# Kernel tuning notes

Hardware: AMD Instinct MI355X
Metric: run time of the kernel (lower is better)

## Reference

```python
import jax, jax.numpy as jnp
import numpy as np

EPS = 1e-5

def _conv1x1(x, w, b):
    # x: (B,C,H,W), w: (O,C), b: (O,)
    return jnp.einsum('bchw,oc->bohw', x, w) + b[None, :, None, None]

def _maxpool2(x):
    B, C, H, W = x.shape
    return x.reshape(B, C, H // 2, 2, W // 2, 2).max(axis=(3, 5))

def setup_inputs() -> dict:
    key = jax.random.key(0)
    ks = jax.random.split(key, 12)
    B, C, Ci, H, W = 8, 256, 128, 64, 64
    s = lambda k, shape, scale: jax.random.normal(k, shape, jnp.float32) * scale
    return {
        'x': s(ks[0], (B, C, H, W), 1.0),
        'neighborFeat': s(ks[1], (B, C, H, W), 1.0),
        'g_w': s(ks[2], (Ci, C), 0.05), 'g_b': jnp.zeros((Ci,), jnp.float32),
        'theta_w': s(ks[3], (Ci, C), 0.05), 'theta_b': jnp.zeros((Ci,), jnp.float32),
        'phi_w': s(ks[4], (Ci, C), 0.05), 'phi_b': jnp.zeros((Ci,), jnp.float32),
        'w_w': s(ks[5], (C, Ci), 0.05), 'w_b': jnp.zeros((C,), jnp.float32),
        'bn_gamma': s(ks[6], (C,), 0.1) + 1.0,
        'bn_beta': s(ks[7], (C,), 0.1),
        'bn_mean': s(ks[8], (C,), 0.1),
        'bn_var': jax.random.uniform(ks[9], (C,), jnp.float32, 0.5, 1.5),
    }

def reference(x, neighborFeat, g_w, g_b, theta_w, theta_b, phi_w, phi_b,
              w_w, w_b, bn_gamma, bn_beta, bn_mean, bn_var):
    B, C, H, W = x.shape
    Ci = g_w.shape[0]
    # g: conv1x1 on x then maxpool2 -> (B, Nkv, Ci)
    g_x = _maxpool2(_conv1x1(x, g_w, g_b)).reshape(B, Ci, -1).transpose(0, 2, 1)
    # theta: conv1x1 on neighborFeat, full res -> (B, Nq, Ci)
    theta_x = _conv1x1(neighborFeat, theta_w, theta_b).reshape(B, Ci, -1).transpose(0, 2, 1)
    # phi: conv1x1 on neighborFeat then maxpool2 -> (B, Ci, Nkv)
    phi_x = _maxpool2(_conv1x1(neighborFeat, phi_w, phi_b)).reshape(B, Ci, -1)
    f = jnp.einsum('bqc,bck->bqk', theta_x, phi_x)       # (B, Nq, Nkv)
    f_div_C = jax.nn.softmax(f, axis=-1)
    y = jnp.einsum('bqk,bkc->bqc', f_div_C, g_x)          # (B, Nq, Ci)
    y = y.transpose(0, 2, 1).reshape(B, Ci, H, W)
    # W: conv1x1 + BatchNorm (eval mode with running stats)
    wy = _conv1x1(y, w_w, w_b)
    wy = (wy - bn_mean[None, :, None, None]) * (bn_gamma[None, :, None, None]
          * jax.lax.rsqrt(bn_var + EPS)[None, :, None, None]) + bn_beta[None, :, None, None]
    return wy + x
```

## Files before the change

kernel.cpp:

```cpp
#include <hip/hip_runtime.h>

typedef __attribute__((ext_vector_type(8))) short short8;
typedef __attribute__((ext_vector_type(4))) short short4v;
typedef __attribute__((ext_vector_type(4))) float f32x4;

__device__ __forceinline__ float bf2f(short s) {
  union { unsigned u; float f; } cv;
  cv.u = ((unsigned)(unsigned short)s) << 16;
  return cv.f;
}
__device__ __forceinline__ short f2bf(float f) {
  union { float f; unsigned u; } cv;
  cv.f = f;
  unsigned r = (cv.u + 0x7fffu + ((cv.u >> 16) & 1u)) >> 16;
  return (short)(unsigned short)r;
}

#define MFMA16(a, b, c) __builtin_amdgcn_mfma_f32_16x16x32_bf16((a), (b), (c), 0, 0, 0)

__global__ __launch_bounds__(256) void cvt_w(
    const float* __restrict__ s0, const float* __restrict__ s1,
    const float* __restrict__ s2, const float* __restrict__ s3,
    short* __restrict__ d)
{
  const float* srcs[4] = {s0, s1, s2, s3};
  const float* s = srcs[blockIdx.y];
  int i = (blockIdx.x * 256 + threadIdx.x) * 4;
  f32x4 v = *reinterpret_cast<const f32x4*>(s + i);
  short4v o;
  #pragma unroll
  for (int j = 0; j < 4; j++) o[j] = f2bf(v[j]);
  *reinterpret_cast<short4v*>(d + (size_t)blockIdx.y * 32768 + i) = o;
}

template <int NPROJ, int MODE1>
__global__ __launch_bounds__(512) void conv_proj(
    const float* __restrict__ in,
    const short* __restrict__ w0, const float* __restrict__ bias0,
    const short* __restrict__ w1, const float* __restrict__ bias1,
    short* __restrict__ out0, short* __restrict__ out1)
{
  __shared__ short in_t[128][40];
  __shared__ short wt[NPROJ][128][40];

  const int b = blockIdx.y;
  const int p0 = blockIdx.x * 128;
  const int tid = threadIdx.x;
  const int wave = tid >> 6, lane = tid & 63;
  const int lr = lane & 15, lg = lane >> 4;

  const short* wsrc[2] = {w0, w1};

  f32x4 acc[NPROJ][8];
  #pragma unroll
  for (int pj = 0; pj < NPROJ; pj++)
    #pragma unroll
    for (int n = 0; n < 8; n++) acc[pj][n] = (f32x4)0.0f;

  for (int kc = 0; kc < 256; kc += 32) {
    __syncthreads();
    {
      int c = tid >> 4;
      int pg = (tid & 15) * 8;
      const float* src = in + ((size_t)(b * 256 + kc + c)) * 4096 + p0 + pg;
      f32x4 v0 = *reinterpret_cast<const f32x4*>(src);
      f32x4 v1 = *reinterpret_cast<const f32x4*>(src + 4);
      #pragma unroll
      for (int j = 0; j < 8; j++) {
        int p = pg + j;
        int a = ((p & 63) >> 1) * 4 + ((p >> 6) << 1) + (p & 1);
        float fv = (j < 4) ? v0[j] : v1[j - 4];
        in_t[a][c ^ ((((a >> 3) & 3)) << 3)] = f2bf(fv);
      }
    }
    if (tid < NPROJ * 128) {
      int pj = tid >> 7, o = tid & 127;
      const short8* src = reinterpret_cast<const short8*>(wsrc[pj] + (size_t)o * 256 + kc);
      int f = (o >> 3) & 3;
      #pragma unroll
      for (int gq = 0; gq < 4; gq++)
        *reinterpret_cast<short8*>(&wt[pj][o][(gq ^ f) * 8]) = src[gq];
    }
    __syncthreads();

    int arow = wave * 16 + lr;
    short8 afrag = *reinterpret_cast<const short8*>(
        &in_t[arow][(lg ^ ((arow >> 3) & 3)) * 8]);
    #pragma unroll
    for (int pj = 0; pj < NPROJ; pj++) {
      #pragma unroll
      for (int n = 0; n < 8; n++) {
        int brow = n * 16 + lr;
        short8 bfrag = *reinterpret_cast<const short8*>(
            &wt[pj][brow][(lg ^ ((brow >> 3) & 3)) * 8]);
        acc[pj][n] = MFMA16(afrag, bfrag, acc[pj][n]);
      }
    }
  }

  const float* bsrc[2] = {bias0, bias1};
  short* osrc[2] = {out0, out1};
  const int kp = blockIdx.x * 32 + wave * 4 + lg;
  #pragma unroll
  for (int pj = 0; pj < NPROJ; pj++) {
    const int mode = (pj == 0 && NPROJ == 2) ? 0 : MODE1;
    #pragma unroll
    for (int n = 0; n < 8; n++) {
      int o = n * 16 + lr;
      float bv = bsrc[pj][o];
      if (mode == 0) {
        #pragma unroll
        for (int r = 0; r < 4; r++) {
          int pix = (wave * 4 + lg) * 2 + (r & 1) + ((r >> 1) & 1) * 64;
          osrc[pj][((size_t)b * 4096 + p0 + pix) * 128 + o] = f2bf(acc[pj][n][r] + bv);
        }
      } else {
        f32x4 v = acc[pj][n];
        float pv = fmaxf(fmaxf(v[0], v[1]), fmaxf(v[2], v[3])) + bv;
        if (mode == 1)
          osrc[pj][((size_t)b * 1024 + kp) * 128 + o] = f2bf(pv);
        else
          osrc[pj][((size_t)b * 128 + o) * 1024 + kp] = f2bf(pv);
      }
    }
  }
}

__global__ __launch_bounds__(512) void attn_split(
    const short* __restrict__ theta, const short* __restrict__ phi,
    const short* __restrict__ g,
    short* __restrict__ pacc0, short* __restrict__ pacc1,
    float* __restrict__ pm, float* __restrict__ pl)
{
  __shared__ short phi_s[64][128];
  __shared__ short g_s[128][64];
  __shared__ short p_s[8][32][64];

  const int b = blockIdx.y;
  const int q0 = blockIdx.x * 256;
  const int z = blockIdx.z;
  const int tid = threadIdx.x;
  const int wave = tid >> 6, lane = tid & 63;
  const int lr = lane & 15, lg = lane >> 4;

  short8 ath[2][4];
  {
    const short* tq = theta + ((size_t)b * 4096 + q0 + wave * 32 + lr) * 128 + lg * 8;
    #pragma unroll
    for (int qh = 0; qh < 2; qh++)
      #pragma unroll
      for (int kk = 0; kk < 4; kk++)
        ath[qh][kk] = *reinterpret_cast<const short8*>(tq + qh * 16 * 128 + kk * 32);
  }

  const int pr = tid >> 3, pc2 = (tid & 7) * 2;
  const int gr = tid >> 2, gc2 = (tid & 3) * 2;
  const short* phi_src = phi + ((size_t)b * 1024 + z * 512 + pr) * 128 + pc2 * 8;
  const short* g_src   = g + ((size_t)b * 128 + gr) * 1024 + z * 512 + gc2 * 8;

  short8 sphi[2], sg[2];
  #pragma unroll
  for (int j = 0; j < 2; j++) {
    sphi[j] = *reinterpret_cast<const short8*>(phi_src + j * 8);
    sg[j]   = *reinterpret_cast<const short8*>(g_src + j * 8);
  }

  float mrun[2] = {-1e30f, -1e30f}, lpart[2] = {0.0f, 0.0f};
  f32x4 acc[2][8];
  #pragma unroll
  for (int qh = 0; qh < 2; qh++)
    #pragma unroll
    for (int n = 0; n < 8; n++) acc[qh][n] = (f32x4)0.0f;

  char* const phib = (char*)&phi_s[0][0];
  char* const gbse = (char*)&g_s[0][0];
  char* const pbase = (char*)&p_s[wave][0][0];
  const int pkey = (lr & 7) << 4;

  for (int t = 0; t < 8; t++) {
    #pragma unroll
    for (int j = 0; j < 2; j++) {
      *reinterpret_cast<short8*>(phib + pr * 256 + (((pc2 + j) ^ (pr & 15)) * 16)) = sphi[j];
      *reinterpret_cast<short8*>(gbse + gr * 128 + (((gc2 + j) ^ (gr & 7)) * 16)) = sg[j];
    }
    __syncthreads();

    if (t < 7) {
      const short* ps = phi_src + (t + 1) * 64 * 128;
      const short* gs = g_src + (t + 1) * 64;
      #pragma unroll
      for (int j = 0; j < 2; j++) {
        sphi[j] = *reinterpret_cast<const short8*>(ps + j * 8);
        sg[j]   = *reinterpret_cast<const short8*>(gs + j * 8);
      }
    }

    f32x4 facc[2][4];
    #pragma unroll
    for (int qh = 0; qh < 2; qh++)
      #pragma unroll
      for (int n = 0; n < 4; n++) facc[qh][n] = (f32x4)0.0f;
    __builtin_amdgcn_s_setprio(1);
    #pragma unroll
    for (int kk = 0; kk < 4; kk++) {
      #pragma unroll
      for (int n = 0; n < 4; n++) {
        int row = n * 16 + lr;
        short8 pf = *reinterpret_cast<const short8*>(
            phib + row * 256 + (((4 * kk + lg) ^ (row & 15)) * 16));
        facc[0][n] = MFMA16(pf, ath[0][kk], facc[0][n]);
        facc[1][n] = MFMA16(pf, ath[1][kk], facc[1][n]);
      }
    }
    __builtin_amdgcn_s_setprio(0);

    float pmax[2];
    #pragma unroll
    for (int qh = 0; qh < 2; qh++) {
      float m0 = fmaxf(fmaxf(facc[qh][0][0], facc[qh][0][1]), fmaxf(facc[qh][0][2], facc[qh][0][3]));
      float m1 = fmaxf(fmaxf(facc[qh][1][0], facc[qh][1][1]), fmaxf(facc[qh][1][2], facc[qh][1][3]));
      float m2 = fmaxf(fmaxf(facc[qh][2][0], facc[qh][2][1]), fmaxf(facc[qh][2][2], facc[qh][2][3]));
      float m3 = fmaxf(fmaxf(facc[qh][3][0], facc[qh][3][1]), fmaxf(facc[qh][3][2], facc[qh][3][3]));
      float m = fmaxf(fmaxf(m0, m1), fmaxf(m2, m3));
      m = fmaxf(m, __shfl_xor(m, 16));
      m = fmaxf(m, __shfl_xor(m, 32));
      pmax[qh] = m;
    }
    bool need = (pmax[0] - mrun[0] > 10.0f) | (pmax[1] - mrun[1] > 10.0f);
    if (__any(need)) {
      float mn0 = fmaxf(mrun[0], pmax[0]);
      float mn1 = fmaxf(mrun[1], pmax[1]);
      float sc0 = __expf(mrun[0] - mn0);
      float sc1 = __expf(mrun[1] - mn1);
      mrun[0] = mn0; mrun[1] = mn1;
      lpart[0] *= sc0; lpart[1] *= sc1;
      #pragma unroll
      for (int r = 0; r < 4; r++) {
        float s0 = __shfl(sc0, lg * 4 + r);
        float s1 = __shfl(sc1, lg * 4 + r);
        #pragma unroll
        for (int n = 0; n < 8; n++) { acc[0][n][r] *= s0; acc[1][n][r] *= s1; }
      }
    }
    #pragma unroll
    for (int qh = 0; qh < 2; qh++) {
      #pragma unroll
      for (int n = 0; n < 4; n++) {
        float e0 = __expf(facc[qh][n][0] - mrun[qh]);
        float e1 = __expf(facc[qh][n][1] - mrun[qh]);
        float e2 = __expf(facc[qh][n][2] - mrun[qh]);
        float e3 = __expf(facc[qh][n][3] - mrun[qh]);
        lpart[qh] += (e0 + e1) + (e2 + e3);
        short4v pk;
        pk[0] = f2bf(e0); pk[1] = f2bf(e1); pk[2] = f2bf(e2); pk[3] = f2bf(e3);
        *reinterpret_cast<short4v*>(
            pbase + (qh * 16 + lr) * 128 + ((n * 32 + lg * 8) ^ pkey)) = pk;
      }
    }

    __builtin_amdgcn_s_setprio(1);
    #pragma unroll
    for (int kk = 0; kk < 2; kk++) {
      short8 pa0 = *reinterpret_cast<const short8*>(
          pbase + lr * 128 + ((kk * 64 + lg * 16) ^ pkey));
      short8 pa1 = *reinterpret_cast<const short8*>(
          pbase + (16 + lr) * 128 + ((kk * 64 + lg * 16) ^ pkey));
      #pragma unroll
      for (int n = 0; n < 8; n++) {
        int row = n * 16 + lr;
        short8 gf = *reinterpret_cast<const short8*>(
            gbse + row * 128 + (((4 * kk + lg) ^ (row & 7)) * 16));
        acc[0][n] = MFMA16(pa0, gf, acc[0][n]);
        acc[1][n] = MFMA16(pa1, gf, acc[1][n]);
      }
    }
    __builtin_amdgcn_s_setprio(0);
    __syncthreads();
  }

  float lsum[2];
  #pragma unroll
  for (int qh = 0; qh < 2; qh++) {
    float s = lpart[qh];
    s += __shfl_xor(s, 16);
    s += __shfl_xor(s, 32);
    lsum[qh] = s;
  }
  if (lane < 16) {
    #pragma unroll
    for (int qh = 0; qh < 2; qh++) {
      int q = q0 + wave * 32 + qh * 16 + lr;
      pm[z * 32768 + b * 4096 + q] = mrun[qh];
      pl[z * 32768 + b * 4096 + q] = lsum[qh];
    }
  }
  short* pacc = z ? pacc1 : pacc0;
  #pragma unroll
  for (int qh = 0; qh < 2; qh++) {
    #pragma unroll
    for (int n = 0; n < 8; n++) {
      #pragma unroll
      for (int r = 0; r < 4; r++) {
        int q = q0 + wave * 32 + qh * 16 + lg * 4 + r;
        pacc[((size_t)b * 4096 + q) * 128 + n * 16 + lr] = f2bf(acc[qh][n][r]);
      }
    }
  }
}

__global__ __launch_bounds__(512) void wconv_bn(
    const short* __restrict__ a0, const short* __restrict__ a1,
    const float* __restrict__ pm, const float* __restrict__ pl,
    const short* __restrict__ ww, const float* __restrict__ wb,
    const float* __restrict__ gamma, const float* __restrict__ beta,
    const float* __restrict__ mean, const float* __restrict__ var,
    const float* __restrict__ x, float* __restrict__ out)
{
  __shared__ short y_s[128][136];
  __shared__ float sc_s[256];
  __shared__ float sh_s[256];

  const int b = blockIdx.y;
  const int q0 = blockIdx.x * 128;
  const int tid = threadIdx.x;
  const int wave = tid >> 6, lane = tid & 63;
  const int lr = lane & 15, lg = lane >> 4;

  {
    int r = tid >> 2, c0 = (tid & 3) * 32;
    int iq = b * 4096 + q0 + r;
    float m0 = pm[iq], m1 = pm[32768 + iq];
    float l0 = pl[iq], l1 = pl[32768 + iq];
    float M = fmaxf(m0, m1);
    float w0 = __expf(m0 - M), w1 = __expf(m1 - M);
    float inv = 1.0f / (w0 * l0 + w1 * l1);
    w0 *= inv; w1 *= inv;
    size_t base = (size_t)iq * 128 + c0;
    #pragma unroll
    for (int j = 0; j < 4; j++) {
      short8 A0 = *reinterpret_cast<const short8*>(a0 + base + j * 8);
      short8 A1 = *reinterpret_cast<const short8*>(a1 + base + j * 8);
      short8 o;
      #pragma unroll
      for (int e = 0; e < 8; e++)
        o[e] = f2bf(w0 * bf2f(A0[e]) + w1 * bf2f(A1[e]));
      *reinterpret_cast<short8*>(&y_s[r][c0 + j * 8]) = o;
    }
    if (tid < 256) {
      float s = gamma[tid] * rsqrtf(var[tid] + 1e-5f);
      sc_s[tid] = s;
      sh_s[tid] = (wb[tid] - mean[tid]) * s + beta[tid];
    }
  }
  __syncthreads();

  f32x4 acc[2][8];
  #pragma unroll
  for (int m = 0; m < 2; m++)
    #pragma unroll
    for (int n = 0; n < 8; n++) acc[m][n] = (f32x4)0.0f;

  #pragma unroll
  for (int kk = 0; kk < 4; kk++) {
    short8 af[2], bfr[8];
    #pragma unroll
    for (int m = 0; m < 2; m++)
      af[m] = *reinterpret_cast<const short8*>(
          ww + (size_t)(wave * 32 + m * 16 + lr) * 128 + kk * 32 + lg * 8);
    #pragma unroll
    for (int n = 0; n < 8; n++)
      bfr[n] = *reinterpret_cast<const short8*>(&y_s[n * 16 + lr][kk * 32 + lg * 8]);
    #pragma unroll
    for (int m = 0; m < 2; m++)
      #pragma unroll
      for (int n = 0; n < 8; n++)
        acc[m][n] = MFMA16(af[m], bfr[n], acc[m][n]);
  }

  #pragma unroll
  for (int m = 0; m < 2; m++) {
    #pragma unroll
    for (int n = 0; n < 8; n++) {
      #pragma unroll
      for (int r = 0; r < 4; r++) {
        int co = wave * 32 + m * 16 + lg * 4 + r;
        int q = q0 + n * 16 + lr;
        size_t oidx = ((size_t)b * 256 + co) * 4096 + q;
        float v = acc[m][n][r] * sc_s[co] + sh_s[co];
        out[oidx] = v + x[oidx];
      }
    }
  }
}

extern "C" void kernel_launch(void* const* d_in, const int* in_sizes, int n_in,
                              void* d_out, int out_size, void* d_ws, size_t ws_size,
                              hipStream_t stream)
{
  const float* x    = (const float*)d_in[0];
  const float* nb   = (const float*)d_in[1];
  const float* g_w  = (const float*)d_in[2];
  const float* g_b  = (const float*)d_in[3];
  const float* th_w = (const float*)d_in[4];
  const float* th_b = (const float*)d_in[5];
  const float* ph_w = (const float*)d_in[6];
  const float* ph_b = (const float*)d_in[7];
  const float* w_w  = (const float*)d_in[8];
  const float* w_b  = (const float*)d_in[9];
  const float* gam  = (const float*)d_in[10];
  const float* bet  = (const float*)d_in[11];
  const float* mu   = (const float*)d_in[12];
  const float* var  = (const float*)d_in[13];
  float* out = (float*)d_out;

  char* ws = (char*)d_ws;
  short* theta_full = (short*)(ws);
  short* pacc0      = (short*)(ws + (size_t)(8u << 20));
  short* pacc1      = (short*)(ws + (size_t)(16u << 20));
  short* phi_kc     = (short*)(ws + (size_t)(24u << 20));
  short* g_ck       = (short*)(ws + (size_t)(26u << 20));
  short* wts        = (short*)(ws + (size_t)(36u << 20));
  float* pm         = (float*)(ws + (size_t)(37u << 20));
  float* pl         = (float*)(ws + (size_t)(38u << 20));
  short* th_wb = wts;
  short* ph_wb = wts + 32768;
  short* g_wb  = wts + 2 * 32768;
  short* w_wb  = wts + 3 * 32768;

  cvt_w<<<dim3(32, 4), 256, 0, stream>>>(th_w, ph_w, g_w, w_w, wts);
  conv_proj<2, 1><<<dim3(32, 8), 512, 0, stream>>>(nb, th_wb, th_b, ph_wb, ph_b,
                                                   theta_full, phi_kc);
  conv_proj<1, 2><<<dim3(32, 8), 512, 0, stream>>>(x, g_wb, g_b, nullptr, nullptr,
                                                   g_ck, nullptr);
  attn_split<<<dim3(16, 8, 2), 512, 0, stream>>>(theta_full, phi_kc, g_ck,
                                                 pacc0, pacc1, pm, pl);
  wconv_bn<<<dim3(32, 8), 512, 0, stream>>>(pacc0, pacc1, pm, pl,
                                            w_wb, w_b, gam, bet, mu, var, x, out);
}
```

Baseline: 91.85 us.

## Switch attention kernel to 32x32 MFMA with register-shuffled P and double-buffered LDS

Rewrites the attention split kernel to use 32x32x16 bf16 MFMA instead of 16x16x32, so each wave handles 32 queries as one tile. The softmax probabilities are rearranged into MFMA operand layout with cross-lane shuffles instead of a round trip through a per-wave LDS buffer. The phi/g LDS tiles are double-buffered, which removes one barrier per iteration. In exchange, LDS use for phi/g doubles and the shuffle and select logic adds ALU work, which could affect occupancy and register pressure.

```diff
diff --git a/kernel.cpp b/kernel.cpp
--- a/kernel.cpp
+++ b/kernel.cpp
@@ -3,6 +3,8 @@
 typedef __attribute__((ext_vector_type(8))) short short8;
 typedef __attribute__((ext_vector_type(4))) short short4v;
 typedef __attribute__((ext_vector_type(4))) float f32x4;
+typedef __attribute__((ext_vector_type(16))) float f32x16;
+typedef __attribute__((ext_vector_type(4))) unsigned u32x4;
 
 __device__ __forceinline__ float bf2f(short s) {
   union { unsigned u; float f; } cv;
@@ -15,8 +17,12 @@
   unsigned r = (cv.u + 0x7fffu + ((cv.u >> 16) & 1u)) >> 16;
   return (short)(unsigned short)r;
 }
+__device__ __forceinline__ unsigned pk2(float a, float b) {
+  return (unsigned)(unsigned short)f2bf(a) | ((unsigned)(unsigned short)f2bf(b) << 16);
+}
 
 #define MFMA16(a, b, c) __builtin_amdgcn_mfma_f32_16x16x32_bf16((a), (b), (c), 0, 0, 0)
+#define MFMA32(a, b, c) __builtin_amdgcn_mfma_f32_32x32x16_bf16((a), (b), (c), 0, 0, 0)
 
 __global__ __launch_bounds__(256) void cvt_w(
     const float* __restrict__ s0, const float* __restrict__ s1,
@@ -132,25 +138,21 @@
     short* __restrict__ pacc0, short* __restrict__ pacc1,
     float* __restrict__ pm, float* __restrict__ pl)
 {
-  __shared__ short phi_s[64][128];
-  __shared__ short g_s[128][64];
-  __shared__ short p_s[8][32][64];
-
-  const int b = blockIdx.y;
+  __shared__ short phi_s[2][64][128];
+  __shared__ short g_s[2][128][64];
+
+  const int b = blockIdx.y, z = blockIdx.z;
   const int q0 = blockIdx.x * 256;
-  const int z = blockIdx.z;
   const int tid = threadIdx.x;
   const int wave = tid >> 6, lane = tid & 63;
-  const int lr = lane & 15, lg = lane >> 4;
-
-  short8 ath[2][4];
+  const int l31 = lane & 31, hi = lane >> 5;
+
+  short8 ath[8];
   {
-    const short* tq = theta + ((size_t)b * 4096 + q0 + wave * 32 + lr) * 128 + lg * 8;
-    #pragma unroll
-    for (int qh = 0; qh < 2; qh++)
-      #pragma unroll
-      for (int kk = 0; kk < 4; kk++)
-        ath[qh][kk] = *reinterpret_cast<const short8*>(tq + qh * 16 * 128 + kk * 32);
+    const short* tq = theta + ((size_t)b * 4096 + q0 + wave * 32 + l31) * 128 + hi * 8;
+    #pragma unroll
+    for (int s = 0; s < 8; s++)
+      ath[s] = *reinterpret_cast<const short8*>(tq + s * 16);
   }
 
   const int pr = tid >> 3, pc2 = (tid & 7) * 2;
@@ -165,25 +167,25 @@
     sg[j]   = *reinterpret_cast<const short8*>(g_src + j * 8);
   }
 
-  float mrun[2] = {-1e30f, -1e30f}, lpart[2] = {0.0f, 0.0f};
-  f32x4 acc[2][8];
-  #pragma unroll
-  for (int qh = 0; qh < 2; qh++)
-    #pragma unroll
-    for (int n = 0; n < 8; n++) acc[qh][n] = (f32x4)0.0f;
-
-  char* const phib = (char*)&phi_s[0][0];
-  char* const gbse = (char*)&g_s[0][0];
-  char* const pbase = (char*)&p_s[wave][0][0];
-  const int pkey = (lr & 7) << 4;
+  float mrun = -1e30f, lpart = 0.0f;
+  f32x16 acc[4];
+  #pragma unroll
+  for (int n = 0; n < 4; n++) acc[n] = (f32x16)0.0f;
+
+  {
+    char* pb = (char*)&phi_s[0][0][0];
+    char* gb = (char*)&g_s[0][0][0];
+    #pragma unroll
+    for (int j = 0; j < 2; j++) {
+      *reinterpret_cast<short8*>(pb + pr * 256 + (((pc2 + j) ^ (pr & 15)) * 16)) = sphi[j];
+      *reinterpret_cast<short8*>(gb + gr * 128 + (((gc2 + j) ^ (gr & 7)) * 16)) = sg[j];
+    }
+  }
 
   for (int t = 0; t < 8; t++) {
-    #pragma unroll
-    for (int j = 0; j < 2; j++) {
-      *reinterpret_cast<short8*>(phib + pr * 256 + (((pc2 + j) ^ (pr & 15)) * 16)) = sphi[j];
-      *reinterpret_cast<short8*>(gbse + gr * 128 + (((gc2 + j) ^ (gr & 7)) * 16)) = sg[j];
-    }
     __syncthreads();
+    char* pb = (char*)&phi_s[t & 1][0][0];
+    char* gb = (char*)&g_s[t & 1][0][0];
 
     if (t < 7) {
       const short* ps = phi_src + (t + 1) * 64 * 128;
@@ -195,115 +197,104 @@
       }
     }
 
-    f32x4 facc[2][4];
-    #pragma unroll
-    for (int qh = 0; qh < 2; qh++)
-      #pragma unroll
-      for (int n = 0; n < 4; n++) facc[qh][n] = (f32x4)0.0f;
+    f32x16 facc0 = (f32x16)0.0f, facc1 = (f32x16)0.0f;
     __builtin_amdgcn_s_setprio(1);
     #pragma unroll
-    for (int kk = 0; kk < 4; kk++) {
+    for (int s = 0; s < 8; s++) {
+      int slot = (s << 1) | hi;
+      short8 pf0 = *reinterpret_cast<const short8*>(
+          pb + l31 * 256 + ((slot ^ (l31 & 15)) * 16));
+      short8 pf1 = *reinterpret_cast<const short8*>(
+          pb + (32 + l31) * 256 + ((slot ^ (l31 & 15)) * 16));
+      facc0 = MFMA32(pf0, ath[s], facc0);
+      facc1 = MFMA32(pf1, ath[s], facc1);
+    }
+    __builtin_amdgcn_s_setprio(0);
+
+    float m = facc0[0];
+    #pragma unroll
+    for (int r = 1; r < 16; r++) m = fmaxf(m, facc0[r]);
+    #pragma unroll
+    for (int r = 0; r < 16; r++) m = fmaxf(m, facc1[r]);
+    m = fmaxf(m, __shfl_xor(m, 32));
+    if (__any(m - mrun > 10.0f)) {
+      float mn = fmaxf(mrun, m);
+      float sc = __expf(mrun - mn);
+      mrun = mn;
+      lpart *= sc;
+      #pragma unroll
+      for (int reg = 0; reg < 16; reg++) {
+        int qr = (reg & 3) + 8 * (reg >> 2) + 4 * hi;
+        float sr = __shfl(sc, qr);
+        #pragma unroll
+        for (int n = 0; n < 4; n++) acc[n][reg] *= sr;
+      }
+    }
+    float ls = 0.0f;
+    #pragma unroll
+    for (int r = 0; r < 16; r++) { facc0[r] = __expf(facc0[r] - mrun); ls += facc0[r]; }
+    #pragma unroll
+    for (int r = 0; r < 16; r++) { facc1[r] = __expf(facc1[r] - mrun); ls += facc1[r]; }
+    lpart += ls;
+
+    __builtin_amdgcn_s_setprio(1);
+    #pragma unroll
+    for (int s = 0; s < 4; s++) {
+      const int base = (s & 1) * 8;
+      float p0, p1, p2, p3, p4, p5, p6, p7;
+      if (s < 2) {
+        p0 = facc0[base + 0]; p1 = facc0[base + 1]; p2 = facc0[base + 2]; p3 = facc0[base + 3];
+        p4 = facc0[base + 4]; p5 = facc0[base + 5]; p6 = facc0[base + 6]; p7 = facc0[base + 7];
+      } else {
+        p0 = facc1[base + 0]; p1 = facc1[base + 1]; p2 = facc1[base + 2]; p3 = facc1[base + 3];
+        p4 = facc1[base + 4]; p5 = facc1[base + 5]; p6 = facc1[base + 6]; p7 = facc1[base + 7];
+      }
+      unsigned P0w0 = pk2(p0, p1), P0w1 = pk2(p2, p3);
+      unsigned P1w0 = pk2(p4, p5), P1w1 = pk2(p6, p7);
+      unsigned x0 = (unsigned)__shfl_xor((int)P0w0, 32);
+      unsigned x1 = (unsigned)__shfl_xor((int)P0w1, 32);
+      unsigned y0 = (unsigned)__shfl_xor((int)P1w0, 32);
+      unsigned y1 = (unsigned)__shfl_xor((int)P1w1, 32);
+      union { u32x4 u; short8 s8; } pf;
+      pf.u[0] = hi ? y0 : P0w0;
+      pf.u[1] = hi ? y1 : P0w1;
+      pf.u[2] = hi ? P1w0 : x0;
+      pf.u[3] = hi ? P1w1 : x1;
+      int slot = (s << 1) | hi;
       #pragma unroll
       for (int n = 0; n < 4; n++) {
-        int row = n * 16 + lr;
-        short8 pf = *reinterpret_cast<const short8*>(
-            phib + row * 256 + (((4 * kk + lg) ^ (row & 15)) * 16));
-        facc[0][n] = MFMA16(pf, ath[0][kk], facc[0][n]);
-        facc[1][n] = MFMA16(pf, ath[1][kk], facc[1][n]);
+        int rg = n * 32 + l31;
+        short8 gf = *reinterpret_cast<const short8*>(
+            gb + rg * 128 + ((slot ^ (rg & 7)) * 16));
+        acc[n] = MFMA32(pf.s8, gf, acc[n]);
       }
     }
     __builtin_amdgcn_s_setprio(0);
 
-    float pmax[2];
-    #pragma unroll
-    for (int qh = 0; qh < 2; qh++) {
-      float m0 = fmaxf(fmaxf(facc[qh][0][0], facc[qh][0][1]), fmaxf(facc[qh][0][2], facc[qh][0][3]));
-      float m1 = fmaxf(fmaxf(facc[qh][1][0], facc[qh][1][1]), fmaxf(facc[qh][1][2], facc[qh][1][3]));
-      float m2 = fmaxf(fmaxf(facc[qh][2][0], facc[qh][2][1]), fmaxf(facc[qh][2][2], facc[qh][2][3]));
-      float m3 = fmaxf(fmaxf(facc[qh][3][0], facc[qh][3][1]), fmaxf(facc[qh][3][2], facc[qh][3][3]));
-      float m = fmaxf(fmaxf(m0, m1), fmaxf(m2, m3));
-      m = fmaxf(m, __shfl_xor(m, 16));
-      m = fmaxf(m, __shfl_xor(m, 32));
-      pmax[qh] = m;
-    }
-    bool need = (pmax[0] - mrun[0] > 10.0f) | (pmax[1] - mrun[1] > 10.0f);
-    if (__any(need)) {
-      float mn0 = fmaxf(mrun[0], pmax[0]);
-      float mn1 = fmaxf(mrun[1], pmax[1]);
-      float sc0 = __expf(mrun[0] - mn0);
-      float sc1 = __expf(mrun[1] - mn1);
-      mrun[0] = mn0; mrun[1] = mn1;
-      lpart[0] *= sc0; lpart[1] *= sc1;
-      #pragma unroll
-      for (int r = 0; r < 4; r++) {
-        float s0 = __shfl(sc0, lg * 4 + r);
-        float s1 = __shfl(sc1, lg * 4 + r);
-        #pragma unroll
-        for (int n = 0; n < 8; n++) { acc[0][n][r] *= s0; acc[1][n][r] *= s1; }
-      }
-    }
-    #pragma unroll
-    for (int qh = 0; qh < 2; qh++) {
-      #pragma unroll
-      for (int n = 0; n < 4; n++) {
-        float e0 = __expf(facc[qh][n][0] - mrun[qh]);
-        float e1 = __expf(facc[qh][n][1] - mrun[qh]);
-        float e2 = __expf(facc[qh][n][2] - mrun[qh]);
-        float e3 = __expf(facc[qh][n][3] - mrun[qh]);
-        lpart[qh] += (e0 + e1) + (e2 + e3);
-        short4v pk;
-        pk[0] = f2bf(e0); pk[1] = f2bf(e1); pk[2] = f2bf(e2); pk[3] = f2bf(e3);
-        *reinterpret_cast<short4v*>(
-            pbase + (qh * 16 + lr) * 128 + ((n * 32 + lg * 8) ^ pkey)) = pk;
-      }
-    }
-
-    __builtin_amdgcn_s_setprio(1);
-    #pragma unroll
-    for (int kk = 0; kk < 2; kk++) {
-      short8 pa0 = *reinterpret_cast<const short8*>(
-          pbase + lr * 128 + ((kk * 64 + lg * 16) ^ pkey));
-      short8 pa1 = *reinterpret_cast<const short8*>(
-          pbase + (16 + lr) * 128 + ((kk * 64 + lg * 16) ^ pkey));
-      #pragma unroll
-      for (int n = 0; n < 8; n++) {
-        int row = n * 16 + lr;
-        short8 gf = *reinterpret_cast<const short8*>(
-            gbse + row * 128 + (((4 * kk + lg) ^ (row & 7)) * 16));
-        acc[0][n] = MFMA16(pa0, gf, acc[0][n]);
-        acc[1][n] = MFMA16(pa1, gf, acc[1][n]);
-      }
-    }
-    __builtin_amdgcn_s_setprio(0);
-    __syncthreads();
-  }
-
-  float lsum[2];
-  #pragma unroll
-  for (int qh = 0; qh < 2; qh++) {
-    float s = lpart[qh];
-    s += __shfl_xor(s, 16);
-    s += __shfl_xor(s, 32);
-    lsum[qh] = s;
-  }
-  if (lane < 16) {
-    #pragma unroll
-    for (int qh = 0; qh < 2; qh++) {
-      int q = q0 + wave * 32 + qh * 16 + lr;
-      pm[z * 32768 + b * 4096 + q] = mrun[qh];
-      pl[z * 32768 + b * 4096 + q] = lsum[qh];
-    }
+    if (t < 7) {
+      char* pb2 = (char*)&phi_s[(t + 1) & 1][0][0];
+      char* gb2 = (char*)&g_s[(t + 1) & 1][0][0];
+      #pragma unroll
+      for (int j = 0; j < 2; j++) {
+        *reinterpret_cast<short8*>(pb2 + pr * 256 + (((pc2 + j) ^ (pr & 15)) * 16)) = sphi[j];
+        *reinterpret_cast<short8*>(gb2 + gr * 128 + (((gc2 + j) ^ (gr & 7)) * 16)) = sg[j];
+      }
+    }
+  }
+
+  float lsum = lpart + __shfl_xor(lpart, 32);
+  if (lane < 32) {
+    int q = q0 + wave * 32 + l31;
+    pm[z * 32768 + b * 4096 + q] = mrun;
+    pl[z * 32768 + b * 4096 + q] = lsum;
   }
   short* pacc = z ? pacc1 : pacc0;
   #pragma unroll
-  for (int qh = 0; qh < 2; qh++) {
-    #pragma unroll
-    for (int n = 0; n < 8; n++) {
-      #pragma unroll
-      for (int r = 0; r < 4; r++) {
-        int q = q0 + wave * 32 + qh * 16 + lg * 4 + r;
-        pacc[((size_t)b * 4096 + q) * 128 + n * 16 + lr] = f2bf(acc[qh][n][r]);
-      }
+  for (int n = 0; n < 4; n++) {
+    #pragma unroll
+    for (int reg = 0; reg < 16; reg++) {
+      int q = q0 + wave * 32 + (reg & 3) + 8 * (reg >> 2) + 4 * hi;
+      pacc[((size_t)b * 4096 + q) * 128 + n * 32 + l31] = f2bf(acc[n][reg]);
     }
   }
 }
```

Result: faster. 89.35 us (-2.7%).
